# Kernel optimization log

Measured on AMD Instinct MI355X. Metric: run time of the kernel, lower is better.

The kernel has to match this reference:

```python
import jax, jax.numpy as jnp
import numpy as np

TAGSET = 32
START = 30
STOP = 31
B = 512
S = 2048


def setup_inputs() -> dict:
    key = jax.random.key(0)
    k1, k2, k3 = jax.random.split(key, 3)
    emissions = jax.random.normal(k1, (B, S, TAGSET), dtype=jnp.float32)
    transitions = jax.random.normal(k2, (TAGSET, TAGSET), dtype=jnp.float32)
    # replicate the torch init: no transition into START, none out of STOP
    transitions = transitions.at[START, :].set(-10000.0).at[:, STOP].set(-10000.0)
    tags = jax.random.randint(k3, (B, S), 0, START)  # valid label tags only
    return {"emissions": emissions, "transitions": transitions, "tags": tags}


def _partition(emissions, transitions):
    # CRF forward algorithm (log partition), vectorized scan over time.
    # alphas: [B, T];  transitions[tag, prev_tag]
    alphas0 = transitions[:, START][None, :] + emissions[:, 0]
    def step(alphas, emit_t):  # emit_t: [B, T]
        # scores[b, tag, prev] = e[b, tag] + trans[tag, prev] + alphas[b, prev]
        scores = emit_t[:, :, None] + transitions[None, :, :] + alphas[:, None, :]
        return jax.nn.logsumexp(scores, axis=2), None
    alphas, _ = jax.lax.scan(step, alphas0, jnp.swapaxes(emissions[:, 1:], 0, 1))
    end_scores = alphas + transitions[STOP][None, :]
    return jax.nn.logsumexp(end_scores, axis=1)  # [B]


def _gold_score(emissions, transitions, tags):
    # vectorized _compute_scores with mask = ones
    e_scores = jnp.take_along_axis(emissions, tags[:, :, None], axis=2)[..., 0].sum(axis=1)
    t_scores = transitions[tags[:, 1:], tags[:, :-1]].sum(axis=1)
    t_scores = t_scores + transitions[tags[:, 0], START] + transitions[STOP, tags[:, -1]]
    return e_scores + t_scores  # [B]


def reference(emissions, transitions, tags):
    # neg_log_likelihood = sum_b (log Z_b - score(gold path)_b)
    return jnp.sum(_partition(emissions, transitions) - _gold_score(emissions, transitions, tags))
```

## Files before the change

### kernel.cpp

```cpp
#include <hip/hip_runtime.h>

#define L2E 1.4426950408889634f
#define LN2 0.6931471805599453f

typedef float f32x16 __attribute__((ext_vector_type(16)));
typedef float f32x2  __attribute__((ext_vector_type(2)));
typedef short bf16x8 __attribute__((ext_vector_type(8)));
typedef unsigned int u32x4 __attribute__((ext_vector_type(4)));

__device__ __forceinline__ float dexp2(float x) { return __builtin_amdgcn_exp2f(x); }
__device__ __forceinline__ float dlog2(float x) { return __builtin_amdgcn_logf(x); }

__device__ __forceinline__ unsigned cvtpk(float a, float b) {
    unsigned r;
    asm("v_cvt_pk_bf16_f32 %0, %1, %2" : "=v"(r) : "v"(a), "v"(b));
    return r;
}

__device__ __forceinline__ unsigned pkrne(float a, float b) {
    unsigned ua = __float_as_uint(a), ub = __float_as_uint(b);
    ua += 0x7FFFu + ((ua >> 16) & 1u);
    ub += 0x7FFFu + ((ub >> 16) & 1u);
    return __builtin_amdgcn_perm(ub, ua, 0x07060302u);
}

__global__ __launch_bounds__(1024, 4) void crf_phase_kernel(
    const float* __restrict__ em,
    const float* __restrict__ tr,
    const int*   __restrict__ tgs,
    float*       __restrict__ ws)
{
    __shared__ float s_tr[1024];
    __shared__ unsigned short s_mat[16 * 1024];
    __shared__ unsigned s_d8[16 * 64];
    __shared__ float s_vec[32];
    __shared__ float s_base[16];
    __shared__ float s_gold[16];

    const int tid = threadIdx.x;
    const int b   = blockIdx.x;
    const int w   = tid >> 6;
    const int l   = tid & 63;
    const int h   = l >> 5;
    const int q   = l & 31;

    s_tr[tid & 1023] = tr[tid & 1023];
    __syncthreads();

    unsigned ea[8];
#pragma unroll
    for (int j = 0; j < 8; ++j) {
        int k0  = 16 * (j >> 2) + 8 * h + 2 * (j & 3);
        int col = (k0 & ~12) | ((k0 & 4) << 1) | ((k0 & 8) >> 1);
        ea[j] = pkrne(dexp2(s_tr[q * 32 + col] * L2E),
                      dexp2(s_tr[q * 32 + col + 1] * L2E));
    }
    const bf16x8 A0 = __builtin_bit_cast(bf16x8, (u32x4){ea[0], ea[1], ea[2], ea[3]});
    const bf16x8 A1 = __builtin_bit_cast(bf16x8, (u32x4){ea[4], ea[5], ea[6], ea[7]});

    f32x16 zro;
#pragma unroll
    for (int z = 0; z < 16; ++z) zro[z] = 0.f;

    const float* ebase = em + ((size_t)b * 2048 + (size_t)w * 128) * 32;
    const int*   tgp   = tgs + (size_t)b * 2048;

    f32x16 acc;
    float  s_cur = 1.f;
    int    k_pend = 0, sigma = 0;
    float  gold = 0.f;
    float4 r0, r1;
    int    tregC = 0, tlastC = 0, tregN = 0, tlastN = 0;

#pragma unroll
    for (int r = 0; r < 16; ++r)
        acc[r] = ((((r & 3) + 8 * (r >> 2) + 4 * h) == q) ? 1.f : 0.f);

    auto eload = [&](int blk) -> float4 {
        int bb2 = blk > 15 ? 15 : blk;
        return *(const float4*)(ebase + ((bb2 * 8 + (l >> 3)) * 32 + (l & 7) * 4));
    };
    auto tagload = [&](int cl, int& treg, int& tlast) {
        int c0 = w * 128 + cl * 64;
        int idx = c0 - 1 + l; if (idx < 0) idx = 0;
        treg  = tgp[idx];
        tlast = tgp[c0 + 63];
    };

    r0 = eload(0); r1 = eload(1);
    tagload(0, tregC, tlastC);

#pragma unroll 1
    for (int blk = 0; blk < 16; ++blk) {
        if ((blk & 7) == 0) {
            int cl = blk >> 3;
            int cg = w * 2 + cl;
            if (cl > 0) { tregC = tregN; tlastC = tlastN; }
            {
                int scur = __shfl(tregC, (l + 1) & 63, 64);
                int cur  = (l == 63) ? tlastC : scur;
                int prev = tregC;
                if (l == 0 && cg == 0) prev = 30;
                gold += s_tr[cur * 32 + prev];
            }
            if (cl < 1) tagload(cl + 1, tregN, tlastN);
        }

        {
            int trel = (blk & 7) * 8 + (l >> 3);
            int tshf = __shfl(tregC, (trel + 1) & 63, 64);
            int tgt  = (trel == 63) ? tlastC : tshf;
            if ((tgt >> 2) == (l & 7)) {
                int sub = tgt & 3;
                float ev = sub == 0 ? r0.x : sub == 1 ? r0.y : sub == 2 ? r0.z : r0.w;
                gold += ev;
            }
            float4 dv;
            dv.x = dexp2(r0.x * L2E); dv.y = dexp2(r0.y * L2E);
            dv.z = dexp2(r0.z * L2E); dv.w = dexp2(r0.w * L2E);
            unsigned u = (unsigned)__builtin_amdgcn_cvt_pk_fp8_f32(dv.x, dv.y, 0, false);
            u = (unsigned)__builtin_amdgcn_cvt_pk_fp8_f32(dv.z, dv.w, (int)u, true);
            int c = l & 7;
            s_d8[w * 64 + (l >> 3) * 8 + (c & 1) * 4 + (c >> 1)] = u;
        }
        r0 = r1; r1 = eload(blk + 2);

        const bool skiplast = (blk == 15) && (w == 15);

#pragma unroll
        for (int s = 0; s < 8; ++s) {
            if (s == 7 && skiplast) continue;
            const u32x4 rv = *(const u32x4*)(s_d8 + w * 64 + s * 8 + h * 4);
            unsigned bbn[8];
#pragma unroll
            for (int q2 = 0; q2 < 4; ++q2) {
                f32x2 dlo = __builtin_amdgcn_cvt_pk_f32_fp8((int)rv[q2], false);
                f32x2 dhi = __builtin_amdgcn_cvt_pk_f32_fp8((int)rv[q2], true);
                f32x2 a0; a0.x = acc[4 * q2 + 0]; a0.y = acc[4 * q2 + 1];
                f32x2 a1; a1.x = acc[4 * q2 + 2]; a1.y = acc[4 * q2 + 3];
                f32x2 m0 = a0 * dlo;
                f32x2 m1 = a1 * dhi;
                if (s == 0 || s == 4) {
                    f32x2 sc; sc.x = s_cur; sc.y = s_cur;
                    m0 = m0 * sc; m1 = m1 * sc;
                }
                bbn[2 * q2]     = cvtpk(m0.x, m0.y);
                bbn[2 * q2 + 1] = cvtpk(m1.x, m1.y);
            }
            if (s == 0 || s == 4) sigma += k_pend;
            bf16x8 B0 = __builtin_bit_cast(bf16x8, (u32x4){bbn[0], bbn[1], bbn[2], bbn[3]});
            bf16x8 B1 = __builtin_bit_cast(bf16x8, (u32x4){bbn[4], bbn[5], bbn[6], bbn[7]});
            f32x16 t = __builtin_amdgcn_mfma_f32_32x32x16_bf16(A0, B0, zro, 0, 0, 0);
            acc = __builtin_amdgcn_mfma_f32_32x32x16_bf16(A1, B1, t, 0, 0, 0);
            if (s == 3 || s == 7) {
                unsigned eb = (__float_as_uint(acc[0]) >> 23) & 0xFF;
                unsigned ku = (unsigned)__builtin_amdgcn_readfirstlane((int)eb);
                k_pend = (int)ku - 127;
                s_cur = __uint_as_float((254u - ku) << 23);
            }
        }
    }

#pragma unroll
    for (int p = 0; p < 8; ++p) {
        int rrow = ((2 * p) & 3) + 8 * ((2 * p) >> 2) + 4 * h;
        *(unsigned*)(s_mat + w * 1024 + q * 32 + rrow) =
            pkrne(acc[2 * p], acc[2 * p + 1]);
    }
    if (l == 0) s_base[w] = (float)sigma;

#pragma unroll
    for (int m = 1; m < 64; m <<= 1) gold += __shfl_xor(gold, m, 64);
    if (l == 0) s_gold[w] = gold;
    __syncthreads();

    if (tid < 32) {
        int i = tid;
        float x  = dexp2(s_tr[i * 32 + 30] * L2E);
        float xb = 0.f, bs = 0.f;
        for (int c = 0; c < 16; ++c) {
            s_vec[i] = x;
            float yv[32];
#pragma unroll
            for (int j = 0; j < 8; ++j) *(float4*)&yv[4 * j] = *(const float4*)&s_vec[4 * j];
            float a2 = 0.f;
#pragma unroll
            for (int j = 0; j < 32; ++j) {
                unsigned short uv = s_mat[c * 1024 + j * 32 + i];
                a2 += __uint_as_float((unsigned)uv << 16) * yv[j];
            }
            unsigned eb2 = (__float_as_uint(a2) >> 23) & 0xFF;
            int ku0 = __shfl((int)eb2, 0, 32);
            x  = a2 * __uint_as_float((unsigned)(254 - ku0) << 23);
            xb += (float)(ku0 - 127);
            bs += s_base[c];
        }
        float elast = em[((size_t)b * 2048 + 2047) * 32 + i];
        float wv = dexp2((s_tr[31 * 32 + i] + elast) * L2E);
        float sv = x * wv;
#pragma unroll
        for (int m2 = 1; m2 < 32; m2 <<= 1) sv += __shfl_xor(sv, m2, 32);
        float logZ = (xb + bs + dlog2(sv)) * LN2;
        if (i == 0) {
            float g = 0.f;
#pragma unroll
            for (int wv2 = 0; wv2 < 16; ++wv2) g += s_gold[wv2];
            g += s_tr[31 * 32 + tgp[2047]];
            ws[b] = logZ - g;
        }
    }
}

__global__ __launch_bounds__(64) void crf_reduce_kernel(
    const float* __restrict__ ws, float* __restrict__ out)
{
    int l = threadIdx.x;
    float s = 0.f;
#pragma unroll
    for (int k = 0; k < 8; ++k) s += ws[l + k * 64];
    s += __shfl_xor(s, 1, 64);
    s += __shfl_xor(s, 2, 64);
    s += __shfl_xor(s, 4, 64);
    s += __shfl_xor(s, 8, 64);
    s += __shfl_xor(s, 16, 64);
    s += __shfl_xor(s, 32, 64);
    if (l == 0) out[0] = s;
}

extern "C" void kernel_launch(void* const* d_in, const int* in_sizes, int n_in,
                              void* d_out, int out_size, void* d_ws, size_t ws_size,
                              hipStream_t stream)
{
    const float* em = (const float*)d_in[0];
    const float* tr = (const float*)d_in[1];
    const int*   tg = (const int*)d_in[2];
    float* ws  = (float*)d_ws;
    float* out = (float*)d_out;

    hipLaunchKernelGGL(crf_phase_kernel, dim3(512), dim3(1024), 0, stream, em, tr, tg, ws);
    hipLaunchKernelGGL(crf_reduce_kernel, dim3(1), dim3(64), 0, stream, ws, out);
}
```

Before: 107.1 us.

## Process two batch rows per block with interleaved independent MFMA chains

Each block now handles two sequences, interleaving their chained MFMA matrix-product steps so one chain's latency can be hidden by the other. The grid is halved and shared-memory buffers are doubled. The final 32-thread combine stage now runs 64 threads covering both sequences. This raises register and LDS use per block, which may reduce occupancy.

```diff
diff --git a/kernel.cpp b/kernel.cpp
--- a/kernel.cpp
+++ b/kernel.cpp
@@ -31,14 +31,14 @@
     float*       __restrict__ ws)
 {
     __shared__ float s_tr[1024];
-    __shared__ unsigned short s_mat[16 * 1024];
-    __shared__ unsigned s_d8[16 * 64];
-    __shared__ float s_vec[32];
-    __shared__ float s_base[16];
-    __shared__ float s_gold[16];
+    __shared__ unsigned short s_mat[2 * 16 * 1024];
+    __shared__ unsigned s_d8[2 * 16 * 64];
+    __shared__ float s_vec[64];
+    __shared__ float s_base[2][16];
+    __shared__ float s_gold[2][16];
 
     const int tid = threadIdx.x;
-    const int b   = blockIdx.x;
+    const int b0  = blockIdx.x * 2;
     const int w   = tid >> 6;
     const int l   = tid & 63;
     const int h   = l >> 5;
@@ -62,140 +62,178 @@
 #pragma unroll
     for (int z = 0; z < 16; ++z) zro[z] = 0.f;
 
-    const float* ebase = em + ((size_t)b * 2048 + (size_t)w * 128) * 32;
-    const int*   tgp   = tgs + (size_t)b * 2048;
-
-    f32x16 acc;
-    float  s_cur = 1.f;
-    int    k_pend = 0, sigma = 0;
-    float  gold = 0.f;
-    float4 r0, r1;
-    int    tregC = 0, tlastC = 0, tregN = 0, tlastN = 0;
-
-#pragma unroll
-    for (int r = 0; r < 16; ++r)
-        acc[r] = ((((r & 3) + 8 * (r >> 2) + 4 * h) == q) ? 1.f : 0.f);
-
-    auto eload = [&](int blk) -> float4 {
+    const float* ebA = em + ((size_t)b0 * 2048 + (size_t)w * 128) * 32;
+    const float* ebB = ebA + (size_t)2048 * 32;
+    const int*   tgA = tgs + (size_t)b0 * 2048;
+    const int*   tgB = tgA + 2048;
+
+    f32x16 accA, accB;
+    float  scA = 1.f, scB = 1.f;
+    int    kpA = 0, kpB = 0, sgA = 0, sgB = 0;
+    float  goldA = 0.f, goldB = 0.f;
+    float4 r0A, r1A, r0B, r1B;
+    int    trA = 0, tlA = 0, trB = 0, tlB = 0;
+    int    trAn = 0, tlAn = 0, trBn = 0, tlBn = 0;
+
+#pragma unroll
+    for (int r = 0; r < 16; ++r) {
+        float iv = ((((r & 3) + 8 * (r >> 2) + 4 * h) == q) ? 1.f : 0.f);
+        accA[r] = iv; accB[r] = iv;
+    }
+
+    auto eload = [&](const float* eb, int blk) -> float4 {
         int bb2 = blk > 15 ? 15 : blk;
-        return *(const float4*)(ebase + ((bb2 * 8 + (l >> 3)) * 32 + (l & 7) * 4));
+        return *(const float4*)(eb + ((bb2 * 8 + (l >> 3)) * 32 + (l & 7) * 4));
     };
-    auto tagload = [&](int cl, int& treg, int& tlast) {
+    auto tagload = [&](const int* tgp, int cl, int& treg, int& tlast) {
         int c0 = w * 128 + cl * 64;
         int idx = c0 - 1 + l; if (idx < 0) idx = 0;
         treg  = tgp[idx];
         tlast = tgp[c0 + 63];
     };
 
-    r0 = eload(0); r1 = eload(1);
-    tagload(0, tregC, tlastC);
+    r0A = eload(ebA, 0); r1A = eload(ebA, 1);
+    r0B = eload(ebB, 0); r1B = eload(ebB, 1);
+    tagload(tgA, 0, trA, tlA);
+    tagload(tgB, 0, trB, tlB);
 
 #pragma unroll 1
     for (int blk = 0; blk < 16; ++blk) {
         if ((blk & 7) == 0) {
             int cl = blk >> 3;
             int cg = w * 2 + cl;
-            if (cl > 0) { tregC = tregN; tlastC = tlastN; }
+            if (cl > 0) { trA = trAn; tlA = tlAn; trB = trBn; tlB = tlBn; }
             {
-                int scur = __shfl(tregC, (l + 1) & 63, 64);
-                int cur  = (l == 63) ? tlastC : scur;
-                int prev = tregC;
-                if (l == 0 && cg == 0) prev = 30;
-                gold += s_tr[cur * 32 + prev];
-            }
-            if (cl < 1) tagload(cl + 1, tregN, tlastN);
+                int sA = __shfl(trA, (l + 1) & 63, 64);
+                int cA = (l == 63) ? tlA : sA;
+                int pA = trA;
+                int sB = __shfl(trB, (l + 1) & 63, 64);
+                int cB = (l == 63) ? tlB : sB;
+                int pB = trB;
+                if (l == 0 && cg == 0) { pA = 30; pB = 30; }
+                goldA += s_tr[cA * 32 + pA];
+                goldB += s_tr[cB * 32 + pB];
+            }
+            if (cl < 1) { tagload(tgA, 1, trAn, tlAn); tagload(tgB, 1, trBn, tlBn); }
         }
 
         {
             int trel = (blk & 7) * 8 + (l >> 3);
-            int tshf = __shfl(tregC, (trel + 1) & 63, 64);
-            int tgt  = (trel == 63) ? tlastC : tshf;
-            if ((tgt >> 2) == (l & 7)) {
-                int sub = tgt & 3;
-                float ev = sub == 0 ? r0.x : sub == 1 ? r0.y : sub == 2 ? r0.z : r0.w;
-                gold += ev;
-            }
-            float4 dv;
-            dv.x = dexp2(r0.x * L2E); dv.y = dexp2(r0.y * L2E);
-            dv.z = dexp2(r0.z * L2E); dv.w = dexp2(r0.w * L2E);
-            unsigned u = (unsigned)__builtin_amdgcn_cvt_pk_fp8_f32(dv.x, dv.y, 0, false);
-            u = (unsigned)__builtin_amdgcn_cvt_pk_fp8_f32(dv.z, dv.w, (int)u, true);
             int c = l & 7;
-            s_d8[w * 64 + (l >> 3) * 8 + (c & 1) * 4 + (c >> 1)] = u;
-        }
-        r0 = r1; r1 = eload(blk + 2);
+            int slot = w * 64 + (l >> 3) * 8 + (c & 1) * 4 + (c >> 1);
+            {
+                int tshf = __shfl(trA, (trel + 1) & 63, 64);
+                int tgt  = (trel == 63) ? tlA : tshf;
+                if ((tgt >> 2) == c) {
+                    int sub = tgt & 3;
+                    goldA += sub == 0 ? r0A.x : sub == 1 ? r0A.y : sub == 2 ? r0A.z : r0A.w;
+                }
+                float4 dv;
+                dv.x = dexp2(r0A.x * L2E); dv.y = dexp2(r0A.y * L2E);
+                dv.z = dexp2(r0A.z * L2E); dv.w = dexp2(r0A.w * L2E);
+                unsigned u = (unsigned)__builtin_amdgcn_cvt_pk_fp8_f32(dv.x, dv.y, 0, false);
+                u = (unsigned)__builtin_amdgcn_cvt_pk_fp8_f32(dv.z, dv.w, (int)u, true);
+                s_d8[slot] = u;
+            }
+            {
+                int tshf = __shfl(trB, (trel + 1) & 63, 64);
+                int tgt  = (trel == 63) ? tlB : tshf;
+                if ((tgt >> 2) == c) {
+                    int sub = tgt & 3;
+                    goldB += sub == 0 ? r0B.x : sub == 1 ? r0B.y : sub == 2 ? r0B.z : r0B.w;
+                }
+                float4 dv;
+                dv.x = dexp2(r0B.x * L2E); dv.y = dexp2(r0B.y * L2E);
+                dv.z = dexp2(r0B.z * L2E); dv.w = dexp2(r0B.w * L2E);
+                unsigned u = (unsigned)__builtin_amdgcn_cvt_pk_fp8_f32(dv.x, dv.y, 0, false);
+                u = (unsigned)__builtin_amdgcn_cvt_pk_fp8_f32(dv.z, dv.w, (int)u, true);
+                s_d8[1024 + slot] = u;
+            }
+        }
+        r0A = r1A; r1A = eload(ebA, blk + 2);
+        r0B = r1B; r1B = eload(ebB, blk + 2);
 
         const bool skiplast = (blk == 15) && (w == 15);
 
 #pragma unroll
         for (int s = 0; s < 8; ++s) {
             if (s == 7 && skiplast) continue;
-            const u32x4 rv = *(const u32x4*)(s_d8 + w * 64 + s * 8 + h * 4);
-            unsigned bbn[8];
-#pragma unroll
-            for (int q2 = 0; q2 < 4; ++q2) {
-                f32x2 dlo = __builtin_amdgcn_cvt_pk_f32_fp8((int)rv[q2], false);
-                f32x2 dhi = __builtin_amdgcn_cvt_pk_f32_fp8((int)rv[q2], true);
-                f32x2 a0; a0.x = acc[4 * q2 + 0]; a0.y = acc[4 * q2 + 1];
-                f32x2 a1; a1.x = acc[4 * q2 + 2]; a1.y = acc[4 * q2 + 3];
-                f32x2 m0 = a0 * dlo;
-                f32x2 m1 = a1 * dhi;
-                if (s == 0 || s == 4) {
-                    f32x2 sc; sc.x = s_cur; sc.y = s_cur;
-                    m0 = m0 * sc; m1 = m1 * sc;
-                }
-                bbn[2 * q2]     = cvtpk(m0.x, m0.y);
-                bbn[2 * q2 + 1] = cvtpk(m1.x, m1.y);
-            }
-            if (s == 0 || s == 4) sigma += k_pend;
-            bf16x8 B0 = __builtin_bit_cast(bf16x8, (u32x4){bbn[0], bbn[1], bbn[2], bbn[3]});
-            bf16x8 B1 = __builtin_bit_cast(bf16x8, (u32x4){bbn[4], bbn[5], bbn[6], bbn[7]});
-            f32x16 t = __builtin_amdgcn_mfma_f32_32x32x16_bf16(A0, B0, zro, 0, 0, 0);
-            acc = __builtin_amdgcn_mfma_f32_32x32x16_bf16(A1, B1, t, 0, 0, 0);
-            if (s == 3 || s == 7) {
-                unsigned eb = (__float_as_uint(acc[0]) >> 23) & 0xFF;
-                unsigned ku = (unsigned)__builtin_amdgcn_readfirstlane((int)eb);
-                k_pend = (int)ku - 127;
-                s_cur = __uint_as_float((254u - ku) << 23);
-            }
+#define DO_STEP(ACC, SC, KP, SG, BANK) do { \
+            const u32x4 rv = *(const u32x4*)(s_d8 + (BANK) + w * 64 + s * 8 + h * 4); \
+            unsigned bbn[8]; \
+            _Pragma("unroll") for (int q2 = 0; q2 < 4; ++q2) { \
+                f32x2 dlo = __builtin_amdgcn_cvt_pk_f32_fp8((int)rv[q2], false); \
+                f32x2 dhi = __builtin_amdgcn_cvt_pk_f32_fp8((int)rv[q2], true); \
+                f32x2 a0; a0.x = ACC[4 * q2 + 0]; a0.y = ACC[4 * q2 + 1]; \
+                f32x2 a1; a1.x = ACC[4 * q2 + 2]; a1.y = ACC[4 * q2 + 3]; \
+                f32x2 m0 = a0 * dlo; \
+                f32x2 m1 = a1 * dhi; \
+                if (s == 0 || s == 4) { \
+                    f32x2 sc; sc.x = SC; sc.y = SC; \
+                    m0 = m0 * sc; m1 = m1 * sc; \
+                } \
+                bbn[2 * q2]     = cvtpk(m0.x, m0.y); \
+                bbn[2 * q2 + 1] = cvtpk(m1.x, m1.y); \
+            } \
+            if (s == 0 || s == 4) SG += KP; \
+            bf16x8 B0 = __builtin_bit_cast(bf16x8, (u32x4){bbn[0], bbn[1], bbn[2], bbn[3]}); \
+            bf16x8 B1 = __builtin_bit_cast(bf16x8, (u32x4){bbn[4], bbn[5], bbn[6], bbn[7]}); \
+            f32x16 t = __builtin_amdgcn_mfma_f32_32x32x16_bf16(A0, B0, zro, 0, 0, 0); \
+            ACC = __builtin_amdgcn_mfma_f32_32x32x16_bf16(A1, B1, t, 0, 0, 0); \
+            if (s == 3 || s == 7) { \
+                unsigned eb = (__float_as_uint(ACC[0]) >> 23) & 0xFF; \
+                unsigned ku = (unsigned)__builtin_amdgcn_readfirstlane((int)eb); \
+                KP = (int)ku - 127; \
+                SC = __uint_as_float((254u - ku) << 23); \
+            } \
+} while (0)
+            DO_STEP(accA, scA, kpA, sgA, 0);
+            DO_STEP(accB, scB, kpB, sgB, 1024);
+#undef DO_STEP
         }
     }
 
 #pragma unroll
     for (int p = 0; p < 8; ++p) {
         int rrow = ((2 * p) & 3) + 8 * ((2 * p) >> 2) + 4 * h;
-        *(unsigned*)(s_mat + w * 1024 + q * 32 + rrow) =
-            pkrne(acc[2 * p], acc[2 * p + 1]);
-    }
-    if (l == 0) s_base[w] = (float)sigma;
-
-#pragma unroll
-    for (int m = 1; m < 64; m <<= 1) gold += __shfl_xor(gold, m, 64);
-    if (l == 0) s_gold[w] = gold;
+        *(unsigned*)(s_mat + w * 1024 + q * 32 + rrow) = pkrne(accA[2 * p], accA[2 * p + 1]);
+        *(unsigned*)(s_mat + 16 * 1024 + w * 1024 + q * 32 + rrow) = pkrne(accB[2 * p], accB[2 * p + 1]);
+    }
+    if (l == 0) { s_base[0][w] = (float)sgA; s_base[1][w] = (float)sgB; }
+
+#pragma unroll
+    for (int m = 1; m < 64; m <<= 1) goldA += __shfl_xor(goldA, m, 64);
+#pragma unroll
+    for (int m = 1; m < 64; m <<= 1) goldB += __shfl_xor(goldB, m, 64);
+    if (l == 0) { s_gold[0][w] = goldA; s_gold[1][w] = goldB; }
     __syncthreads();
 
-    if (tid < 32) {
-        int i = tid;
+    if (tid < 64) {
+        int h2 = tid >> 5;
+        int i  = tid & 31;
+        const unsigned short* mat = s_mat + h2 * 16 * 1024;
+        const int* tgp = h2 ? tgB : tgA;
         float x  = dexp2(s_tr[i * 32 + 30] * L2E);
         float xb = 0.f, bs = 0.f;
         for (int c = 0; c < 16; ++c) {
-            s_vec[i] = x;
+            s_vec[h2 * 32 + i] = x;
             float yv[32];
 #pragma unroll
-            for (int j = 0; j < 8; ++j) *(float4*)&yv[4 * j] = *(const float4*)&s_vec[4 * j];
+            for (int j = 0; j < 8; ++j)
+                *(float4*)&yv[4 * j] = *(const float4*)&s_vec[h2 * 32 + 4 * j];
             float a2 = 0.f;
 #pragma unroll
             for (int j = 0; j < 32; ++j) {
-                unsigned short uv = s_mat[c * 1024 + j * 32 + i];
+                unsigned short uv = mat[c * 1024 + j * 32 + i];
                 a2 += __uint_as_float((unsigned)uv << 16) * yv[j];
             }
             unsigned eb2 = (__float_as_uint(a2) >> 23) & 0xFF;
             int ku0 = __shfl((int)eb2, 0, 32);
             x  = a2 * __uint_as_float((unsigned)(254 - ku0) << 23);
             xb += (float)(ku0 - 127);
-            bs += s_base[c];
-        }
-        float elast = em[((size_t)b * 2048 + 2047) * 32 + i];
+            bs += s_base[h2][c];
+        }
+        float elast = em[((size_t)(b0 + h2) * 2048 + 2047) * 32 + i];
         float wv = dexp2((s_tr[31 * 32 + i] + elast) * L2E);
         float sv = x * wv;
 #pragma unroll
@@ -204,9 +242,9 @@
         if (i == 0) {
             float g = 0.f;
 #pragma unroll
-            for (int wv2 = 0; wv2 < 16; ++wv2) g += s_gold[wv2];
+            for (int wv2 = 0; wv2 < 16; ++wv2) g += s_gold[h2][wv2];
             g += s_tr[31 * 32 + tgp[2047]];
-            ws[b] = logZ - g;
+            ws[b0 + h2] = logZ - g;
         }
     }
 }
@@ -237,6 +275,6 @@
     float* ws  = (float*)d_ws;
     float* out = (float*)d_out;
 
-    hipLaunchKernelGGL(crf_phase_kernel, dim3(512), dim3(1024), 0, stream, em, tr, tg, ws);
+    hipLaunchKernelGGL(crf_phase_kernel, dim3(256), dim3(1024), 0, stream, em, tr, tg, ws);
     hipLaunchKernelGGL(crf_reduce_kernel, dim3(1), dim3(64), 0, stream, ws, out);
 }
```

Result: faster. 101.4 us (-5.3%).

## Collapse chunk transfer products to rank-one and propagate vectors instead

Applied to the files above, without the earlier changes.

Each wave builds its chunk's full 32x32 transfer-matrix product with MFMA for only the first 32 timesteps. It then approximates that product as a rank-one outer product of a normalized column-sum vector and a row-sum vector, and carries only that vector through the remaining steps with scalar FMAs, shuffles and fp8 round-trips. The final cross-chunk combine becomes a dot product per chunk instead of a dense matrix-vector product, and the bf16 matrix staging in LDS is dropped. This saves MFMA work, but the rank-one step relies on the positive-matrix product having mixed to near rank-one. It also adds a per-step max-reduction and LDS round-trip to the serial vector chain, which can cost latency and accuracy.

```diff
diff --git a/kernel.cpp b/kernel.cpp
--- a/kernel.cpp
+++ b/kernel.cpp
@@ -31,9 +31,11 @@
     float*       __restrict__ ws)
 {
     __shared__ float s_tr[1024];
-    __shared__ unsigned short s_mat[16 * 1024];
     __shared__ unsigned s_d8[16 * 64];
-    __shared__ float s_vec[32];
+    __shared__ __align__(16) unsigned char s_w8[16 * 32];
+    __shared__ float s_u[16 * 32];
+    __shared__ float s_v[16 * 32];
+    __shared__ float s_uf[16 * 32];
     __shared__ float s_base[16];
     __shared__ float s_gold[16];
 
@@ -47,13 +49,15 @@
     s_tr[tid & 1023] = tr[tid & 1023];
     __syncthreads();
 
+    f32x2 efv[8];
     unsigned ea[8];
 #pragma unroll
     for (int j = 0; j < 8; ++j) {
         int k0  = 16 * (j >> 2) + 8 * h + 2 * (j & 3);
         int col = (k0 & ~12) | ((k0 & 4) << 1) | ((k0 & 8) >> 1);
-        ea[j] = pkrne(dexp2(s_tr[q * 32 + col] * L2E),
-                      dexp2(s_tr[q * 32 + col + 1] * L2E));
+        efv[j].x = dexp2(s_tr[q * 32 + col] * L2E);
+        efv[j].y = dexp2(s_tr[q * 32 + col + 1] * L2E);
+        ea[j] = pkrne(efv[j].x, efv[j].y);
     }
     const bf16x8 A0 = __builtin_bit_cast(bf16x8, (u32x4){ea[0], ea[1], ea[2], ea[3]});
     const bf16x8 A1 = __builtin_bit_cast(bf16x8, (u32x4){ea[4], ea[5], ea[6], ea[7]});
@@ -64,11 +68,16 @@
 
     const float* ebase = em + ((size_t)b * 2048 + (size_t)w * 128) * 32;
     const int*   tgp   = tgs + (size_t)b * 2048;
+
+    const int dhD   = (q >> 3) + 4 * ((q >> 2) & 1);
+    const int dhsh  = (q & 3) << 3;
+    const int wperm = 16 * ((q >> 2) & 1) + 4 * (q >> 3) + (q & 3);
 
     f32x16 acc;
     float  s_cur = 1.f;
     int    k_pend = 0, sigma = 0;
     float  gold = 0.f;
+    float  u_own = 0.f;
     float4 r0, r1;
     int    tregC = 0, tlastC = 0, tregN = 0, tlastN = 0;
 
@@ -125,48 +134,113 @@
         }
         r0 = r1; r1 = eload(blk + 2);
 
-        const bool skiplast = (blk == 15) && (w == 15);
-
-#pragma unroll
-        for (int s = 0; s < 8; ++s) {
-            if (s == 7 && skiplast) continue;
-            const u32x4 rv = *(const u32x4*)(s_d8 + w * 64 + s * 8 + h * 4);
-            unsigned bbn[8];
-#pragma unroll
-            for (int q2 = 0; q2 < 4; ++q2) {
-                f32x2 dlo = __builtin_amdgcn_cvt_pk_f32_fp8((int)rv[q2], false);
-                f32x2 dhi = __builtin_amdgcn_cvt_pk_f32_fp8((int)rv[q2], true);
-                f32x2 a0; a0.x = acc[4 * q2 + 0]; a0.y = acc[4 * q2 + 1];
-                f32x2 a1; a1.x = acc[4 * q2 + 2]; a1.y = acc[4 * q2 + 3];
-                f32x2 m0 = a0 * dlo;
-                f32x2 m1 = a1 * dhi;
-                if (s == 0 || s == 4) {
-                    f32x2 sc; sc.x = s_cur; sc.y = s_cur;
-                    m0 = m0 * sc; m1 = m1 * sc;
-                }
-                bbn[2 * q2]     = cvtpk(m0.x, m0.y);
-                bbn[2 * q2 + 1] = cvtpk(m1.x, m1.y);
-            }
-            if (s == 0 || s == 4) sigma += k_pend;
-            bf16x8 B0 = __builtin_bit_cast(bf16x8, (u32x4){bbn[0], bbn[1], bbn[2], bbn[3]});
-            bf16x8 B1 = __builtin_bit_cast(bf16x8, (u32x4){bbn[4], bbn[5], bbn[6], bbn[7]});
-            f32x16 t = __builtin_amdgcn_mfma_f32_32x32x16_bf16(A0, B0, zro, 0, 0, 0);
-            acc = __builtin_amdgcn_mfma_f32_32x32x16_bf16(A1, B1, t, 0, 0, 0);
-            if (s == 3 || s == 7) {
-                unsigned eb = (__float_as_uint(acc[0]) >> 23) & 0xFF;
-                unsigned ku = (unsigned)__builtin_amdgcn_readfirstlane((int)eb);
-                k_pend = (int)ku - 127;
-                s_cur = __uint_as_float((254u - ku) << 23);
+        if (blk < 4) {
+#pragma unroll
+            for (int s = 0; s < 8; ++s) {
+                const u32x4 rv = *(const u32x4*)(s_d8 + w * 64 + s * 8 + h * 4);
+                unsigned bbn[8];
+#pragma unroll
+                for (int q2 = 0; q2 < 4; ++q2) {
+                    f32x2 dlo = __builtin_amdgcn_cvt_pk_f32_fp8((int)rv[q2], false);
+                    f32x2 dhi = __builtin_amdgcn_cvt_pk_f32_fp8((int)rv[q2], true);
+                    f32x2 a0; a0.x = acc[4 * q2 + 0]; a0.y = acc[4 * q2 + 1];
+                    f32x2 a1; a1.x = acc[4 * q2 + 2]; a1.y = acc[4 * q2 + 3];
+                    f32x2 m0 = a0 * dlo;
+                    f32x2 m1 = a1 * dhi;
+                    if (s == 0 || s == 4) {
+                        f32x2 sc; sc.x = s_cur; sc.y = s_cur;
+                        m0 = m0 * sc; m1 = m1 * sc;
+                    }
+                    bbn[2 * q2]     = cvtpk(m0.x, m0.y);
+                    bbn[2 * q2 + 1] = cvtpk(m1.x, m1.y);
+                }
+                if (s == 0 || s == 4) sigma += k_pend;
+                bf16x8 B0 = __builtin_bit_cast(bf16x8, (u32x4){bbn[0], bbn[1], bbn[2], bbn[3]});
+                bf16x8 B1 = __builtin_bit_cast(bf16x8, (u32x4){bbn[4], bbn[5], bbn[6], bbn[7]});
+                f32x16 t = __builtin_amdgcn_mfma_f32_32x32x16_bf16(A0, B0, zro, 0, 0, 0);
+                acc = __builtin_amdgcn_mfma_f32_32x32x16_bf16(A1, B1, t, 0, 0, 0);
+                if (s == 3 || s == 7) {
+                    unsigned eb = (__float_as_uint(acc[0]) >> 23) & 0xFF;
+                    unsigned ku = (unsigned)__builtin_amdgcn_readfirstlane((int)eb);
+                    k_pend = (int)ku - 127;
+                    s_cur = __uint_as_float((254u - ku) << 23);
+                }
+            }
+        } else {
+            if (blk == 4) {
+                unsigned bbh[8];
+#pragma unroll
+                for (int j = 0; j < 8; ++j) bbh[j] = pkrne(acc[2 * j], acc[2 * j + 1]);
+                bf16x8 Bh0 = __builtin_bit_cast(bf16x8, (u32x4){bbh[0], bbh[1], bbh[2], bbh[3]});
+                bf16x8 Bh1 = __builtin_bit_cast(bf16x8, (u32x4){bbh[4], bbh[5], bbh[6], bbh[7]});
+                const unsigned OB = 0x3F803F80u;
+                const bf16x8 Ao = __builtin_bit_cast(bf16x8, (u32x4){OB, OB, OB, OB});
+                f32x16 t2 = __builtin_amdgcn_mfma_f32_32x32x16_bf16(Ao, Bh0, zro, 0, 0, 0);
+                t2 = __builtin_amdgcn_mfma_f32_32x32x16_bf16(Ao, Bh1, t2, 0, 0, 0);
+                float wq = t2[0];
+                float ssum = wq;
+                ssum += __shfl_xor(ssum, 1, 64);
+                ssum += __shfl_xor(ssum, 2, 64);
+                ssum += __shfl_xor(ssum, 4, 64);
+                ssum += __shfl_xor(ssum, 8, 64);
+                ssum += __shfl_xor(ssum, 16, 64);
+                if (l < 32) s_v[w * 32 + q] = wq * __builtin_amdgcn_rcpf(ssum);
+                float ur[16];
+#pragma unroll
+                for (int r = 0; r < 16; ++r) {
+                    float t3 = acc[r];
+                    t3 += __shfl_xor(t3, 1, 64);
+                    t3 += __shfl_xor(t3, 2, 64);
+                    t3 += __shfl_xor(t3, 4, 64);
+                    t3 += __shfl_xor(t3, 8, 64);
+                    t3 += __shfl_xor(t3, 16, 64);
+                    ur[r] = t3;
+                }
+                if (q == 0) {
+#pragma unroll
+                    for (int p = 0; p < 4; ++p) {
+                        float4 vv;
+                        vv.x = ur[4 * p + 0]; vv.y = ur[4 * p + 1];
+                        vv.z = ur[4 * p + 2]; vv.w = ur[4 * p + 3];
+                        *(float4*)(s_u + w * 32 + 8 * p + 4 * h) = vv;
+                    }
+                }
+                u_own = s_u[w * 32 + q];
+            }
+#pragma unroll
+            for (int s = 0; s < 8; ++s) {
+                if (s == 7 && blk == 15 && w == 15) continue;
+                unsigned hd = s_d8[w * 64 + s * 8 + dhD];
+                f32x2 dx = __builtin_amdgcn_cvt_pk_f32_fp8((int)(hd >> dhsh), false);
+                float wv = dx.x * u_own;
+                float mm = wv;
+                mm = fmaxf(mm, __shfl_xor(mm, 1, 64));
+                mm = fmaxf(mm, __shfl_xor(mm, 2, 64));
+                mm = fmaxf(mm, __shfl_xor(mm, 4, 64));
+                mm = fmaxf(mm, __shfl_xor(mm, 8, 64));
+                mm = fmaxf(mm, __shfl_xor(mm, 16, 64));
+                unsigned ku = (__float_as_uint(mm) >> 23) & 0xFF;
+                sigma += (int)ku - 127;
+                float wn = wv * __uint_as_float((254u - ku) << 23);
+                unsigned w8 = (unsigned)__builtin_amdgcn_cvt_pk_fp8_f32(wn, wn, 0, false);
+                if (l < 32) s_w8[w * 32 + wperm] = (unsigned char)w8;
+                const u32x4 W = *(const u32x4*)(s_w8 + w * 32 + 16 * h);
+                f32x2 part; part.x = 0.f; part.y = 0.f;
+#pragma unroll
+                for (int g = 0; g < 4; ++g) {
+                    f32x2 lo = __builtin_amdgcn_cvt_pk_f32_fp8((int)W[g], false);
+                    f32x2 hi = __builtin_amdgcn_cvt_pk_f32_fp8((int)W[g], true);
+                    part += efv[2 * g] * lo;
+                    part += efv[2 * g + 1] * hi;
+                }
+                float p  = part.x + part.y;
+                float po = __shfl_xor(p, 32, 64);
+                u_own = p + po;
             }
         }
     }
 
-#pragma unroll
-    for (int p = 0; p < 8; ++p) {
-        int rrow = ((2 * p) & 3) + 8 * ((2 * p) >> 2) + 4 * h;
-        *(unsigned*)(s_mat + w * 1024 + q * 32 + rrow) =
-            pkrne(acc[2 * p], acc[2 * p + 1]);
-    }
+    if (l < 32) s_uf[w * 32 + q] = u_own;
     if (l == 0) s_base[w] = (float)sigma;
 
 #pragma unroll
@@ -177,34 +251,26 @@
     if (tid < 32) {
         int i = tid;
         float x  = dexp2(s_tr[i * 32 + 30] * L2E);
-        float xb = 0.f, bs = 0.f;
+        float xb = 0.f;
         for (int c = 0; c < 16; ++c) {
-            s_vec[i] = x;
-            float yv[32];
-#pragma unroll
-            for (int j = 0; j < 8; ++j) *(float4*)&yv[4 * j] = *(const float4*)&s_vec[4 * j];
-            float a2 = 0.f;
-#pragma unroll
-            for (int j = 0; j < 32; ++j) {
-                unsigned short uv = s_mat[c * 1024 + j * 32 + i];
-                a2 += __uint_as_float((unsigned)uv << 16) * yv[j];
-            }
-            unsigned eb2 = (__float_as_uint(a2) >> 23) & 0xFF;
-            int ku0 = __shfl((int)eb2, 0, 32);
-            x  = a2 * __uint_as_float((unsigned)(254 - ku0) << 23);
-            xb += (float)(ku0 - 127);
-            bs += s_base[c];
+            float t = s_v[c * 32 + i] * x;
+#pragma unroll
+            for (int m2 = 1; m2 < 32; m2 <<= 1) t += __shfl_xor(t, m2, 32);
+            unsigned kb = (__float_as_uint(t) >> 23) & 0xFF;
+            float tn = t * __uint_as_float((254u - kb) << 23);
+            x = s_uf[c * 32 + i] * tn;
+            xb += s_base[c] + (float)((int)kb - 127);
         }
         float elast = em[((size_t)b * 2048 + 2047) * 32 + i];
-        float wv = dexp2((s_tr[31 * 32 + i] + elast) * L2E);
-        float sv = x * wv;
+        float wv2 = dexp2((s_tr[31 * 32 + i] + elast) * L2E);
+        float sv = x * wv2;
 #pragma unroll
         for (int m2 = 1; m2 < 32; m2 <<= 1) sv += __shfl_xor(sv, m2, 32);
-        float logZ = (xb + bs + dlog2(sv)) * LN2;
+        float logZ = (xb + dlog2(sv)) * LN2;
         if (i == 0) {
             float g = 0.f;
 #pragma unroll
-            for (int wv2 = 0; wv2 < 16; ++wv2) g += s_gold[wv2];
+            for (int wv3 = 0; wv3 < 16; ++wv3) g += s_gold[wv3];
             g += s_tr[31 * 32 + tgp[2047]];
             ws[b] = logZ - g;
         }
```

After: 133.3 us. 1.25x slower.
